# Optimization experiments

Measured on AMD Instinct MI355X. Metric: run time of the kernel, lower is better.

## Reference

```python
import jax, jax.numpy as jnp
import numpy as np

N = 100000   # nodes
E = 1600000  # edges
IN = 32      # in_dim
D = 64       # embed_dim
G = 128      # num graphs
EPS = 1e-5   # BatchNorm eps


def setup_inputs() -> dict:
    key = jax.random.key(0)
    ks = jax.random.split(key, 12)
    s_in = 1.0 / np.sqrt(IN)
    s_d = 1.0 / np.sqrt(D)
    return {
        "x": jax.random.normal(ks[0], (N, IN), jnp.float32),
        "edge_index": jax.random.randint(ks[1], (2, E), 0, N),
        "batch": jnp.sort(jax.random.randint(ks[2], (N,), 0, G)),
        "W_embed": jax.random.normal(ks[3], (IN, D), jnp.float32) * s_in,
        "W1": jax.random.normal(ks[4], (D, D), jnp.float32) * s_d,
        "b1": jnp.zeros((D,), jnp.float32),
        "g1": jnp.ones((D,), jnp.float32),
        "bt1": jnp.zeros((D,), jnp.float32),
        "W2": jax.random.normal(ks[5], (D, D), jnp.float32) * s_d,
        "b2": jnp.zeros((D,), jnp.float32),
        "g2": jnp.ones((D,), jnp.float32),
        "bt2": jnp.zeros((D,), jnp.float32),
    }


def reference(x, edge_index, batch, W_embed, W1, b1, g1, bt1, W2, b2, g2, bt2):
    src, dst = edge_index[0], edge_index[1]
    # GCN symmetric norm with self loops: deg = in-degree + 1 (self loop)
    deg = jnp.zeros((N,), x.dtype).at[dst].add(1.0) + 1.0
    dis = jax.lax.rsqrt(deg)                      # deg^{-1/2}, [N]
    enorm = dis[src] * dis[dst]                   # per-edge norm, [E]
    self_norm = dis * dis                         # self-loop norm, [N]

    def gcn_bn(h, W, b, g, bt, relu):
        hw = h @ W                                # linear first (GCNConv)
        msg = hw[src] * enorm[:, None]            # [E, D] gather + scale
        agg = jax.ops.segment_sum(msg, dst, num_segments=N)
        agg = agg + hw * self_norm[:, None] + b   # self loops + bias
        # BatchNorm1d (training mode: batch stats, biased var)
        mu = agg.mean(axis=0)
        var = agg.var(axis=0)
        hn = (agg - mu) * jax.lax.rsqrt(var + EPS) * g + bt
        return jnp.maximum(hn, 0.0) if relu else hn

    h = x @ W_embed                               # node_embed (Linear, no bias)
    h = gcn_bn(h, W1, b1, g1, bt1, relu=True)     # ReLU only between layers
    h = gcn_bn(h, W2, b2, g2, bt2, relu=False)
    h_pool = jax.ops.segment_sum(h, batch, num_segments=G)  # global_add_pool
    return (h, h_pool)
```

## Files before the change

kernel.cpp:

```cpp
#include <hip/hip_runtime.h>

#define NN 100000
#define NE 1600000
#define IN_DIM 32
#define DD 64
#define NG 128
#define BN_EPS 1e-5f
#define AGG_BLOCKS 2048

typedef unsigned short ushort_t;
typedef unsigned int uint_t;
typedef __attribute__((ext_vector_type(8))) short bf16x8;
typedef __attribute__((ext_vector_type(4))) float f32x4;

__device__ __forceinline__ ushort_t f2bf(float f) {
    uint_t u = __float_as_uint(f);
    u = (u + 0x7FFFu + ((u >> 16) & 1u)) >> 16;
    return (ushort_t)u;
}
__device__ __forceinline__ uint_t pack2(float a, float b) {
    return (uint_t)f2bf(a) | ((uint_t)f2bf(b) << 16);
}
__device__ __forceinline__ float bflo(uint_t u) { return __uint_as_float(u << 16); }
__device__ __forceinline__ float bfhi(uint_t u) { return __uint_as_float(u & 0xFFFF0000u); }

__global__ void init_k(int* __restrict__ ints, long n_ints, float* __restrict__ pool,
                       float* __restrict__ sums) {
    long i = (long)blockIdx.x * blockDim.x + threadIdx.x;
    if (i < n_ints) ints[i] = 0;
    if (i < (long)NG * DD) pool[i] = 0.f;
    if (i < 256) sums[i] = 0.f;
}

__global__ void deg_rank(const int* __restrict__ dst, int* __restrict__ cnt,
                         int* __restrict__ rank) {
    int e = blockIdx.x * blockDim.x + threadIdx.x;
    if (e < NE) rank[e] = atomicAdd(&cnt[dst[e]], 1);
}

__global__ __launch_bounds__(256) void alloc_k(const int* __restrict__ cnt,
                                               int* __restrict__ start,
                                               int* __restrict__ cursor,
                                               float* __restrict__ dis) {
    __shared__ int ls[256];
    __shared__ int base_s;
    int t = threadIdx.x;
    long n = (long)blockIdx.x * 256 + t;
    int v = (n < NN) ? cnt[n] : 0;
    ls[t] = v;
    __syncthreads();
    for (int off = 1; off < 256; off <<= 1) {
        int y = (t >= off) ? ls[t - off] : 0;
        __syncthreads();
        ls[t] += y;
        __syncthreads();
    }
    if (t == 0) base_s = atomicAdd(cursor, ls[255]);
    __syncthreads();
    if (n < NN) {
        start[n] = base_s + ls[t] - v;
        dis[n] = rsqrtf((float)v + 1.0f);
    }
}

__global__ void fill_edges(const int* __restrict__ src, const int* __restrict__ dstp,
                           const int* __restrict__ rank, const float* __restrict__ dis,
                           const int* __restrict__ start, uint_t* __restrict__ ep) {
    int e = blockIdx.x * blockDim.x + threadIdx.x;
    if (e >= NE) return;
    int s = src[e], t = dstp[e];
    float nm = dis[s] * dis[t];
    uint_t nb = (__float_as_uint(nm) + 0x8000u) >> 16;
    ep[start[t] + rank[e]] = (uint_t)s | ((nb & 0x7FFFu) << 17);
}

__global__ __launch_bounds__(256) void mm1_k(const float* __restrict__ x,
                                             const float* __restrict__ We,
                                             const float* __restrict__ W1,
                                             ushort_t* __restrict__ hwb) {
    __shared__ float W1s[DD * DD];
    __shared__ float Ws[IN_DIM * DD];
    int t = threadIdx.x;
    for (int i = t; i < DD * DD; i += 256) W1s[i] = W1[i];
    __syncthreads();
    for (int idx = t; idx < IN_DIM * DD; idx += 256) {
        int i = idx >> 6, j = idx & 63;
        float s = 0.f;
#pragma unroll
        for (int k = 0; k < DD; ++k) s += We[i * DD + k] * W1s[k * DD + j];
        Ws[idx] = s;
    }
    __syncthreads();
    long n = (long)blockIdx.x * 256 + t;
    if (n >= NN) return;
    float acc[DD];
#pragma unroll
    for (int d = 0; d < DD; ++d) acc[d] = 0.f;
    const float4* xr = (const float4*)(x + n * IN_DIM);
#pragma unroll
    for (int k4 = 0; k4 < IN_DIM / 4; ++k4) {
        float4 xv = xr[k4];
        const float* xp = (const float*)&xv;
#pragma unroll
        for (int kk = 0; kk < 4; ++kk) {
            float v = xp[kk];
            const float4* w4 = (const float4*)&Ws[(k4 * 4 + kk) * DD];
#pragma unroll
            for (int d4 = 0; d4 < DD / 4; ++d4) {
                float4 wv = w4[d4];
                acc[4 * d4 + 0] += v * wv.x;
                acc[4 * d4 + 1] += v * wv.y;
                acc[4 * d4 + 2] += v * wv.z;
                acc[4 * d4 + 3] += v * wv.w;
            }
        }
    }
    uint4* o = (uint4*)(hwb + n * DD);
#pragma unroll
    for (int d8 = 0; d8 < DD / 8; ++d8) {
        uint4 pk;
        pk.x = pack2(acc[8 * d8 + 0], acc[8 * d8 + 1]);
        pk.y = pack2(acc[8 * d8 + 2], acc[8 * d8 + 3]);
        pk.z = pack2(acc[8 * d8 + 4], acc[8 * d8 + 5]);
        pk.w = pack2(acc[8 * d8 + 6], acc[8 * d8 + 7]);
        o[d8] = pk;
    }
}

__global__ __launch_bounds__(256) void mm2_bn_mfma(const ushort_t* __restrict__ aggb,
                                                   const float* __restrict__ sums,
                                                   const float* __restrict__ g,
                                                   const float* __restrict__ bt,
                                                   const float* __restrict__ W,
                                                   ushort_t* __restrict__ hwb) {
    __shared__ ushort_t Wf[2 * 4 * 64 * 8];
    __shared__ float mu_s[DD], sc_s[DD], bt_s[DD];
    int t = threadIdx.x;
    if (t < DD) {
        const float inv_n = 1.0f / (float)NN;
        float mu = sums[t] * inv_n;
        float var = sums[64 + t] * inv_n - mu * mu;
        mu_s[t] = mu;
        sc_s[t] = g[t] * rsqrtf(var + BN_EPS);
        bt_s[t] = bt[t];
    }
    for (int e = t; e < 4096; e += 256) {
        int ks = e >> 11;
        int c = (e >> 9) & 3;
        int l = (e >> 3) & 63;
        int j = e & 7;
        int k = ks * 32 + ((l >> 4) << 3) + j;
        int col = c * 16 + (l & 15);
        Wf[e] = f2bf(W[k * DD + col]);
    }
    __syncthreads();

    int w = t >> 6, l = t & 63;
    int lr = l & 15, lk = l >> 4;

#pragma unroll
    for (int gi = 0; gi < 4; ++gi) {
        long rowbase = (long)blockIdx.x * 256 + w * 64 + gi * 16;
        long r = rowbase + lr;

        bf16x8 afrag[2];
#pragma unroll
        for (int ks = 0; ks < 2; ++ks) {
            int k0 = ks * 32 + (lk << 3);
            uint4 av = (r < NN) ? *(const uint4*)(aggb + r * DD + k0)
                                : make_uint4(0, 0, 0, 0);
            float4 muA = *(const float4*)&mu_s[k0];
            float4 muB = *(const float4*)&mu_s[k0 + 4];
            float4 scA = *(const float4*)&sc_s[k0];
            float4 scB = *(const float4*)&sc_s[k0 + 4];
            float4 btA = *(const float4*)&bt_s[k0];
            float4 btB = *(const float4*)&bt_s[k0 + 4];
            float h0 = fmaxf((bflo(av.x) - muA.x) * scA.x + btA.x, 0.f);
            float h1 = fmaxf((bfhi(av.x) - muA.y) * scA.y + btA.y, 0.f);
            float h2 = fmaxf((bflo(av.y) - muA.z) * scA.z + btA.z, 0.f);
            float h3 = fmaxf((bfhi(av.y) - muA.w) * scA.w + btA.w, 0.f);
            float h4 = fmaxf((bflo(av.z) - muB.x) * scB.x + btB.x, 0.f);
            float h5 = fmaxf((bfhi(av.z) - muB.y) * scB.y + btB.y, 0.f);
            float h6 = fmaxf((bflo(av.w) - muB.z) * scB.z + btB.z, 0.f);
            float h7 = fmaxf((bfhi(av.w) - muB.w) * scB.w + btB.w, 0.f);
            bf16x8 fr;
            fr[0] = (short)f2bf(h0); fr[1] = (short)f2bf(h1);
            fr[2] = (short)f2bf(h2); fr[3] = (short)f2bf(h3);
            fr[4] = (short)f2bf(h4); fr[5] = (short)f2bf(h5);
            fr[6] = (short)f2bf(h6); fr[7] = (short)f2bf(h7);
            afrag[ks] = fr;
        }

        f32x4 acc[4];
#pragma unroll
        for (int c = 0; c < 4; ++c) acc[c] = (f32x4){0.f, 0.f, 0.f, 0.f};
#pragma unroll
        for (int c = 0; c < 4; ++c) {
#pragma unroll
            for (int ks = 0; ks < 2; ++ks) {
                bf16x8 bfr = *(bf16x8*)&Wf[((ks * 4 + c) << 9) + (l << 3)];
                acc[c] = __builtin_amdgcn_mfma_f32_16x16x32_bf16(afrag[ks], bfr, acc[c],
                                                                 0, 0, 0);
            }
        }

#pragma unroll
        for (int c = 0; c < 4; ++c) {
#pragma unroll
            for (int rr = 0; rr < 4; ++rr) {
                long orow = rowbase + lk * 4 + rr;
                if (orow < NN) hwb[orow * DD + c * 16 + lr] = f2bf(acc[c][rr]);
            }
        }
    }
}

template <int WAGG_BF16>
__global__ __launch_bounds__(256) void gcn_agg(const ushort_t* __restrict__ hwb,
                                               const float* __restrict__ dis,
                                               const int* __restrict__ cnt,
                                               const int* __restrict__ start,
                                               const uint_t* __restrict__ ep,
                                               const float* __restrict__ bias,
                                               void* __restrict__ aggv,
                                               float* __restrict__ sums) {
    int t = threadIdx.x;
    int w = t >> 6;
    int lane = t & 63;
    int j = lane >> 3;
    int c = lane & 7;
    float selfmask = (j == 0) ? 1.f : 0.f;

    __shared__ float ls[4][128];
    for (int k = t; k < 512; k += 256) ((float*)ls)[k] = 0.f;
    __syncthreads();

    float bs[8];
#pragma unroll
    for (int k = 0; k < 8; ++k) bs[k] = bias[8 * c + k];

    for (long n = (long)blockIdx.x * 4 + w; n < NN; n += (long)gridDim.x * 4) {
        int rs = start[n];
        int ce = cnt[n];
        float sn = dis[n];
        float sq = sn * sn;

        uint4 sv = ((const uint4*)(hwb + (long)n * DD))[c];
        float acc[8];
        acc[0] = selfmask * (bflo(sv.x) * sq + bs[0]);
        acc[1] = selfmask * (bfhi(sv.x) * sq + bs[1]);
        acc[2] = selfmask * (bflo(sv.y) * sq + bs[2]);
        acc[3] = selfmask * (bfhi(sv.y) * sq + bs[3]);
        acc[4] = selfmask * (bflo(sv.z) * sq + bs[4]);
        acc[5] = selfmask * (bfhi(sv.z) * sq + bs[5]);
        acc[6] = selfmask * (bflo(sv.w) * sq + bs[6]);
        acc[7] = selfmask * (bfhi(sv.w) * sq + bs[7]);

        for (int i = 0; i < ce; i += 32) {
            int i0 = i + j, i1 = i + 8 + j, i2 = i + 16 + j, i3 = i + 24 + j;
            uint_t u0 = (i0 < ce) ? ep[rs + i0] : 0u;
            uint_t u1 = (i1 < ce) ? ep[rs + i1] : 0u;
            uint_t u2 = (i2 < ce) ? ep[rs + i2] : 0u;
            uint_t u3 = (i3 < ce) ? ep[rs + i3] : 0u;
            uint4 q0 = ((const uint4*)(hwb + (long)(u0 & 0x1FFFF) * DD))[c];
            uint4 q1 = ((const uint4*)(hwb + (long)(u1 & 0x1FFFF) * DD))[c];
            uint4 q2 = ((const uint4*)(hwb + (long)(u2 & 0x1FFFF) * DD))[c];
            uint4 q3 = ((const uint4*)(hwb + (long)(u3 & 0x1FFFF) * DD))[c];
            float n0 = __uint_as_float((u0 >> 17) << 16);
            float n1 = __uint_as_float((u1 >> 17) << 16);
            float n2 = __uint_as_float((u2 >> 17) << 16);
            float n3 = __uint_as_float((u3 >> 17) << 16);
            acc[0] += bflo(q0.x) * n0; acc[1] += bfhi(q0.x) * n0;
            acc[2] += bflo(q0.y) * n0; acc[3] += bfhi(q0.y) * n0;
            acc[4] += bflo(q0.z) * n0; acc[5] += bfhi(q0.z) * n0;
            acc[6] += bflo(q0.w) * n0; acc[7] += bfhi(q0.w) * n0;
            acc[0] += bflo(q1.x) * n1; acc[1] += bfhi(q1.x) * n1;
            acc[2] += bflo(q1.y) * n1; acc[3] += bfhi(q1.y) * n1;
            acc[4] += bflo(q1.z) * n1; acc[5] += bfhi(q1.z) * n1;
            acc[6] += bflo(q1.w) * n1; acc[7] += bfhi(q1.w) * n1;
            acc[0] += bflo(q2.x) * n2; acc[1] += bfhi(q2.x) * n2;
            acc[2] += bflo(q2.y) * n2; acc[3] += bfhi(q2.y) * n2;
            acc[4] += bflo(q2.z) * n2; acc[5] += bfhi(q2.z) * n2;
            acc[6] += bflo(q2.w) * n2; acc[7] += bfhi(q2.w) * n2;
            acc[0] += bflo(q3.x) * n3; acc[1] += bfhi(q3.x) * n3;
            acc[2] += bflo(q3.y) * n3; acc[3] += bfhi(q3.y) * n3;
            acc[4] += bflo(q3.z) * n3; acc[5] += bfhi(q3.z) * n3;
            acc[6] += bflo(q3.w) * n3; acc[7] += bfhi(q3.w) * n3;
        }

#pragma unroll
        for (int m = 8; m < 64; m <<= 1) {
#pragma unroll
            for (int k = 0; k < 8; ++k) acc[k] += __shfl_xor(acc[k], m, 64);
        }

        if (j == 0) {
            if (WAGG_BF16) {
                uint4 pk;
                pk.x = pack2(acc[0], acc[1]);
                pk.y = pack2(acc[2], acc[3]);
                pk.z = pack2(acc[4], acc[5]);
                pk.w = pack2(acc[6], acc[7]);
                ((uint4*)((ushort_t*)aggv + (long)n * DD))[c] = pk;
            } else {
                float4* op = (float4*)((float*)aggv + (long)n * DD + 8 * c);
                op[0] = make_float4(acc[0], acc[1], acc[2], acc[3]);
                op[1] = make_float4(acc[4], acc[5], acc[6], acc[7]);
            }
#pragma unroll
            for (int k = 0; k < 8; ++k) {
                ls[w][8 * c + k] += acc[k];
                ls[w][64 + 8 * c + k] += acc[k] * acc[k];
            }
        }
    }

    __syncthreads();
    if (t < 128) {
        float a = ls[0][t] + ls[1][t] + ls[2][t] + ls[3][t];
        atomicAdd(&sums[t], a);
    }
}

__global__ __launch_bounds__(256) void bn_pool(const float* __restrict__ agg,
                                               const float* __restrict__ sums,
                                               const float* __restrict__ g,
                                               const float* __restrict__ bt,
                                               const int* __restrict__ batch,
                                               float* __restrict__ out,
                                               float* __restrict__ pool) {
    int t = threadIdx.x;
    int d = t & 63, rq = t >> 6;
    const float inv_n = 1.0f / (float)NN;
    float mu = sums[d] * inv_n;
    float var = sums[64 + d] * inv_n - mu * mu;
    float sc = g[d] * rsqrtf(var + BN_EPS);
    float bd = bt[d];
    long base = (long)blockIdx.x * 256;
    float acc = 0.f;
    int cur = -1;
    for (int i = 0; i < 64; ++i) {
        long r = base + rq + 4 * i;
        if (r >= NN) break;
        int b = batch[r];
        float v = (agg[r * DD + d] - mu) * sc + bd;
        out[r * DD + d] = v;
        if (b != cur) {
            if (cur >= 0) atomicAdd(&pool[(long)cur * DD + d], acc);
            acc = 0.f;
            cur = b;
        }
        acc += v;
    }
    if (cur >= 0) atomicAdd(&pool[(long)cur * DD + d], acc);
}

extern "C" void kernel_launch(void* const* d_in, const int* in_sizes, int n_in,
                              void* d_out, int out_size, void* d_ws, size_t ws_size,
                              hipStream_t stream) {
    const float* x = (const float*)d_in[0];
    const int* ei = (const int*)d_in[1];
    const int* batch = (const int*)d_in[2];
    const float* W_embed = (const float*)d_in[3];
    const float* W1 = (const float*)d_in[4];
    const float* b1 = (const float*)d_in[5];
    const float* g1 = (const float*)d_in[6];
    const float* bt1 = (const float*)d_in[7];
    const float* W2 = (const float*)d_in[8];
    const float* b2 = (const float*)d_in[9];
    const float* g2 = (const float*)d_in[10];
    const float* bt2 = (const float*)d_in[11];

    const int* src = ei;
    const int* dst = ei + NE;

    float* out = (float*)d_out;
    float* pool = out + (long)NN * DD;

    const long ND = (long)NN * DD;

    char* w = (char*)d_ws;
    int* cnt = (int*)w;           w += sizeof(int) * NN;
    int* cursor = (int*)w;        w += sizeof(int) * 4;
    int* start = (int*)w;         w += sizeof(int) * NN;
    float* dis = (float*)w;       w += sizeof(float) * NN;
    float* sums1 = (float*)w;     w += sizeof(float) * 128;
    float* sums2 = (float*)w;     w += sizeof(float) * 128;
    int* rank = (int*)w;          w += sizeof(int) * NE;
    uint_t* ep = (uint_t*)w;      w += sizeof(uint_t) * NE;
    ushort_t* hwb = (ushort_t*)w; w += sizeof(ushort_t) * ND;
    ushort_t* agg1b = (ushort_t*)w; w += sizeof(ushort_t) * ND;
    float* aggbuf = (float*)w;

    dim3 blk(256);
    const int nbN = (NN + 255) / 256;
    const int nbE = (NE + 255) / 256;
    const long n_ints = (long)NN + 4;

    init_k<<<dim3((int)((n_ints + 255) / 256)), blk, 0, stream>>>(cnt, n_ints, pool, sums1);
    deg_rank<<<dim3(nbE), blk, 0, stream>>>(dst, cnt, rank);
    alloc_k<<<dim3(nbN), blk, 0, stream>>>(cnt, start, cursor, dis);
    fill_edges<<<dim3(nbE), blk, 0, stream>>>(src, dst, rank, dis, start, ep);

    mm1_k<<<dim3(nbN), blk, 0, stream>>>(x, W_embed, W1, hwb);

    gcn_agg<1><<<dim3(AGG_BLOCKS), blk, 0, stream>>>(hwb, dis, cnt, start, ep, b1,
                                                     (void*)agg1b, sums1);

    mm2_bn_mfma<<<dim3(nbN), blk, 0, stream>>>(agg1b, sums1, g1, bt1, W2, hwb);

    gcn_agg<0><<<dim3(AGG_BLOCKS), blk, 0, stream>>>(hwb, dis, cnt, start, ep, b2,
                                                     (void*)aggbuf, sums2);

    bn_pool<<<dim3(nbN), blk, 0, stream>>>(aggbuf, sums2, g2, bt2, batch, out, pool);
}
```

Baseline: 401.2 us.

## Factor GCN symmetric norm into pre/post scaling and drop per-edge weights

Folds dis[src] into the stored node features (scaled in mm1 and mm2 epilogues) and applies dis[dst] once per destination after aggregation, so each edge needs no per-edge norm. The edge list becomes plain source indices, fill_edges no longer gathers dis, and the inner aggregation loop loses its per-edge multiplies and bit-unpacking. Out-of-range lanes now point at an extra zeroed padding row instead of row 0. Rounding changes slightly because the scaled features are stored in bf16 before summation.

```diff
diff --git a/kernel.cpp b/kernel.cpp
--- a/kernel.cpp
+++ b/kernel.cpp
@@ -25,11 +25,12 @@
 __device__ __forceinline__ float bfhi(uint_t u) { return __uint_as_float(u & 0xFFFF0000u); }
 
 __global__ void init_k(int* __restrict__ ints, long n_ints, float* __restrict__ pool,
-                       float* __restrict__ sums) {
+                       float* __restrict__ sums, ushort_t* __restrict__ hwb) {
     long i = (long)blockIdx.x * blockDim.x + threadIdx.x;
     if (i < n_ints) ints[i] = 0;
     if (i < (long)NG * DD) pool[i] = 0.f;
     if (i < 256) sums[i] = 0.f;
+    if (i < DD) hwb[(long)NN * DD + i] = 0;
 }
 
 __global__ void deg_rank(const int* __restrict__ dst, int* __restrict__ cnt,
@@ -64,19 +65,17 @@
 }
 
 __global__ void fill_edges(const int* __restrict__ src, const int* __restrict__ dstp,
-                           const int* __restrict__ rank, const float* __restrict__ dis,
-                           const int* __restrict__ start, uint_t* __restrict__ ep) {
+                           const int* __restrict__ rank, const int* __restrict__ start,
+                           int* __restrict__ ep) {
     int e = blockIdx.x * blockDim.x + threadIdx.x;
     if (e >= NE) return;
-    int s = src[e], t = dstp[e];
-    float nm = dis[s] * dis[t];
-    uint_t nb = (__float_as_uint(nm) + 0x8000u) >> 16;
-    ep[start[t] + rank[e]] = (uint_t)s | ((nb & 0x7FFFu) << 17);
+    ep[start[dstp[e]] + rank[e]] = src[e];
 }
 
 __global__ __launch_bounds__(256) void mm1_k(const float* __restrict__ x,
                                              const float* __restrict__ We,
                                              const float* __restrict__ W1,
+                                             const float* __restrict__ dis,
                                              ushort_t* __restrict__ hwb) {
     __shared__ float W1s[DD * DD];
     __shared__ float Ws[IN_DIM * DD];
@@ -115,14 +114,15 @@
             }
         }
     }
+    float sn = dis[n];
     uint4* o = (uint4*)(hwb + n * DD);
 #pragma unroll
     for (int d8 = 0; d8 < DD / 8; ++d8) {
         uint4 pk;
-        pk.x = pack2(acc[8 * d8 + 0], acc[8 * d8 + 1]);
-        pk.y = pack2(acc[8 * d8 + 2], acc[8 * d8 + 3]);
-        pk.z = pack2(acc[8 * d8 + 4], acc[8 * d8 + 5]);
-        pk.w = pack2(acc[8 * d8 + 6], acc[8 * d8 + 7]);
+        pk.x = pack2(acc[8 * d8 + 0] * sn, acc[8 * d8 + 1] * sn);
+        pk.y = pack2(acc[8 * d8 + 2] * sn, acc[8 * d8 + 3] * sn);
+        pk.z = pack2(acc[8 * d8 + 4] * sn, acc[8 * d8 + 5] * sn);
+        pk.w = pack2(acc[8 * d8 + 6] * sn, acc[8 * d8 + 7] * sn);
         o[d8] = pk;
     }
 }
@@ -132,6 +132,7 @@
                                                    const float* __restrict__ g,
                                                    const float* __restrict__ bt,
                                                    const float* __restrict__ W,
+                                                   const float* __restrict__ dis,
                                                    ushort_t* __restrict__ hwb) {
     __shared__ ushort_t Wf[2 * 4 * 64 * 8];
     __shared__ float mu_s[DD], sc_s[DD], bt_s[DD];
@@ -205,11 +206,13 @@
         }
 
 #pragma unroll
-        for (int c = 0; c < 4; ++c) {
-#pragma unroll
-            for (int rr = 0; rr < 4; ++rr) {
-                long orow = rowbase + lk * 4 + rr;
-                if (orow < NN) hwb[orow * DD + c * 16 + lr] = f2bf(acc[c][rr]);
+        for (int rr = 0; rr < 4; ++rr) {
+            long orow = rowbase + lk * 4 + rr;
+            if (orow < NN) {
+                float sn = dis[orow];
+#pragma unroll
+                for (int c = 0; c < 4; ++c)
+                    hwb[orow * DD + c * 16 + lr] = f2bf(acc[c][rr] * sn);
             }
         }
     }
@@ -220,7 +223,7 @@
                                                const float* __restrict__ dis,
                                                const int* __restrict__ cnt,
                                                const int* __restrict__ start,
-                                               const uint_t* __restrict__ ep,
+                                               const int* __restrict__ ep,
                                                const float* __restrict__ bias,
                                                void* __restrict__ aggv,
                                                float* __restrict__ sums) {
@@ -242,50 +245,44 @@
     for (long n = (long)blockIdx.x * 4 + w; n < NN; n += (long)gridDim.x * 4) {
         int rs = start[n];
         int ce = cnt[n];
-        float sn = dis[n];
-        float sq = sn * sn;
 
         uint4 sv = ((const uint4*)(hwb + (long)n * DD))[c];
         float acc[8];
-        acc[0] = selfmask * (bflo(sv.x) * sq + bs[0]);
-        acc[1] = selfmask * (bfhi(sv.x) * sq + bs[1]);
-        acc[2] = selfmask * (bflo(sv.y) * sq + bs[2]);
-        acc[3] = selfmask * (bfhi(sv.y) * sq + bs[3]);
-        acc[4] = selfmask * (bflo(sv.z) * sq + bs[4]);
-        acc[5] = selfmask * (bfhi(sv.z) * sq + bs[5]);
-        acc[6] = selfmask * (bflo(sv.w) * sq + bs[6]);
-        acc[7] = selfmask * (bfhi(sv.w) * sq + bs[7]);
+        acc[0] = selfmask * bflo(sv.x);
+        acc[1] = selfmask * bfhi(sv.x);
+        acc[2] = selfmask * bflo(sv.y);
+        acc[3] = selfmask * bfhi(sv.y);
+        acc[4] = selfmask * bflo(sv.z);
+        acc[5] = selfmask * bfhi(sv.z);
+        acc[6] = selfmask * bflo(sv.w);
+        acc[7] = selfmask * bfhi(sv.w);
 
         for (int i = 0; i < ce; i += 32) {
             int i0 = i + j, i1 = i + 8 + j, i2 = i + 16 + j, i3 = i + 24 + j;
-            uint_t u0 = (i0 < ce) ? ep[rs + i0] : 0u;
-            uint_t u1 = (i1 < ce) ? ep[rs + i1] : 0u;
-            uint_t u2 = (i2 < ce) ? ep[rs + i2] : 0u;
-            uint_t u3 = (i3 < ce) ? ep[rs + i3] : 0u;
-            uint4 q0 = ((const uint4*)(hwb + (long)(u0 & 0x1FFFF) * DD))[c];
-            uint4 q1 = ((const uint4*)(hwb + (long)(u1 & 0x1FFFF) * DD))[c];
-            uint4 q2 = ((const uint4*)(hwb + (long)(u2 & 0x1FFFF) * DD))[c];
-            uint4 q3 = ((const uint4*)(hwb + (long)(u3 & 0x1FFFF) * DD))[c];
-            float n0 = __uint_as_float((u0 >> 17) << 16);
-            float n1 = __uint_as_float((u1 >> 17) << 16);
-            float n2 = __uint_as_float((u2 >> 17) << 16);
-            float n3 = __uint_as_float((u3 >> 17) << 16);
-            acc[0] += bflo(q0.x) * n0; acc[1] += bfhi(q0.x) * n0;
-            acc[2] += bflo(q0.y) * n0; acc[3] += bfhi(q0.y) * n0;
-            acc[4] += bflo(q0.z) * n0; acc[5] += bfhi(q0.z) * n0;
-            acc[6] += bflo(q0.w) * n0; acc[7] += bfhi(q0.w) * n0;
-            acc[0] += bflo(q1.x) * n1; acc[1] += bfhi(q1.x) * n1;
-            acc[2] += bflo(q1.y) * n1; acc[3] += bfhi(q1.y) * n1;
-            acc[4] += bflo(q1.z) * n1; acc[5] += bfhi(q1.z) * n1;
-            acc[6] += bflo(q1.w) * n1; acc[7] += bfhi(q1.w) * n1;
-            acc[0] += bflo(q2.x) * n2; acc[1] += bfhi(q2.x) * n2;
-            acc[2] += bflo(q2.y) * n2; acc[3] += bfhi(q2.y) * n2;
-            acc[4] += bflo(q2.z) * n2; acc[5] += bfhi(q2.z) * n2;
-            acc[6] += bflo(q2.w) * n2; acc[7] += bfhi(q2.w) * n2;
-            acc[0] += bflo(q3.x) * n3; acc[1] += bfhi(q3.x) * n3;
-            acc[2] += bflo(q3.y) * n3; acc[3] += bfhi(q3.y) * n3;
-            acc[4] += bflo(q3.z) * n3; acc[5] += bfhi(q3.z) * n3;
-            acc[6] += bflo(q3.w) * n3; acc[7] += bfhi(q3.w) * n3;
+            int u0 = (i0 < ce) ? ep[rs + i0] : NN;
+            int u1 = (i1 < ce) ? ep[rs + i1] : NN;
+            int u2 = (i2 < ce) ? ep[rs + i2] : NN;
+            int u3 = (i3 < ce) ? ep[rs + i3] : NN;
+            uint4 q0 = ((const uint4*)(hwb + (long)u0 * DD))[c];
+            uint4 q1 = ((const uint4*)(hwb + (long)u1 * DD))[c];
+            uint4 q2 = ((const uint4*)(hwb + (long)u2 * DD))[c];
+            uint4 q3 = ((const uint4*)(hwb + (long)u3 * DD))[c];
+            acc[0] += bflo(q0.x); acc[1] += bfhi(q0.x);
+            acc[2] += bflo(q0.y); acc[3] += bfhi(q0.y);
+            acc[4] += bflo(q0.z); acc[5] += bfhi(q0.z);
+            acc[6] += bflo(q0.w); acc[7] += bfhi(q0.w);
+            acc[0] += bflo(q1.x); acc[1] += bfhi(q1.x);
+            acc[2] += bflo(q1.y); acc[3] += bfhi(q1.y);
+            acc[4] += bflo(q1.z); acc[5] += bfhi(q1.z);
+            acc[6] += bflo(q1.w); acc[7] += bfhi(q1.w);
+            acc[0] += bflo(q2.x); acc[1] += bfhi(q2.x);
+            acc[2] += bflo(q2.y); acc[3] += bfhi(q2.y);
+            acc[4] += bflo(q2.z); acc[5] += bfhi(q2.z);
+            acc[6] += bflo(q2.w); acc[7] += bfhi(q2.w);
+            acc[0] += bflo(q3.x); acc[1] += bfhi(q3.x);
+            acc[2] += bflo(q3.y); acc[3] += bfhi(q3.y);
+            acc[4] += bflo(q3.z); acc[5] += bfhi(q3.z);
+            acc[6] += bflo(q3.w); acc[7] += bfhi(q3.w);
         }
 
 #pragma unroll
@@ -295,22 +292,26 @@
         }
 
         if (j == 0) {
+            float sn = dis[n];
+            float v[8];
+#pragma unroll
+            for (int k = 0; k < 8; ++k) v[k] = acc[k] * sn + bs[k];
             if (WAGG_BF16) {
                 uint4 pk;
-                pk.x = pack2(acc[0], acc[1]);
-                pk.y = pack2(acc[2], acc[3]);
-                pk.z = pack2(acc[4], acc[5]);
-                pk.w = pack2(acc[6], acc[7]);
+                pk.x = pack2(v[0], v[1]);
+                pk.y = pack2(v[2], v[3]);
+                pk.z = pack2(v[4], v[5]);
+                pk.w = pack2(v[6], v[7]);
                 ((uint4*)((ushort_t*)aggv + (long)n * DD))[c] = pk;
             } else {
                 float4* op = (float4*)((float*)aggv + (long)n * DD + 8 * c);
-                op[0] = make_float4(acc[0], acc[1], acc[2], acc[3]);
-                op[1] = make_float4(acc[4], acc[5], acc[6], acc[7]);
+                op[0] = make_float4(v[0], v[1], v[2], v[3]);
+                op[1] = make_float4(v[4], v[5], v[6], v[7]);
             }
 #pragma unroll
             for (int k = 0; k < 8; ++k) {
-                ls[w][8 * c + k] += acc[k];
-                ls[w][64 + 8 * c + k] += acc[k] * acc[k];
+                ls[w][8 * c + k] += v[k];
+                ls[w][64 + 8 * c + k] += v[k] * v[k];
             }
         }
     }
@@ -387,8 +388,8 @@
     float* sums1 = (float*)w;     w += sizeof(float) * 128;
     float* sums2 = (float*)w;     w += sizeof(float) * 128;
     int* rank = (int*)w;          w += sizeof(int) * NE;
-    uint_t* ep = (uint_t*)w;      w += sizeof(uint_t) * NE;
-    ushort_t* hwb = (ushort_t*)w; w += sizeof(ushort_t) * ND;
+    int* ep = (int*)w;            w += sizeof(int) * NE;
+    ushort_t* hwb = (ushort_t*)w; w += sizeof(ushort_t) * (ND + DD);
     ushort_t* agg1b = (ushort_t*)w; w += sizeof(ushort_t) * ND;
     float* aggbuf = (float*)w;
 
@@ -397,17 +398,18 @@
     const int nbE = (NE + 255) / 256;
     const long n_ints = (long)NN + 4;
 
-    init_k<<<dim3((int)((n_ints + 255) / 256)), blk, 0, stream>>>(cnt, n_ints, pool, sums1);
+    init_k<<<dim3((int)((n_ints + 255) / 256)), blk, 0, stream>>>(cnt, n_ints, pool,
+                                                                  sums1, hwb);
     deg_rank<<<dim3(nbE), blk, 0, stream>>>(dst, cnt, rank);
     alloc_k<<<dim3(nbN), blk, 0, stream>>>(cnt, start, cursor, dis);
-    fill_edges<<<dim3(nbE), blk, 0, stream>>>(src, dst, rank, dis, start, ep);
-
-    mm1_k<<<dim3(nbN), blk, 0, stream>>>(x, W_embed, W1, hwb);
+    fill_edges<<<dim3(nbE), blk, 0, stream>>>(src, dst, rank, start, ep);
+
+    mm1_k<<<dim3(nbN), blk, 0, stream>>>(x, W_embed, W1, dis, hwb);
 
     gcn_agg<1><<<dim3(AGG_BLOCKS), blk, 0, stream>>>(hwb, dis, cnt, start, ep, b1,
                                                      (void*)agg1b, sums1);
 
-    mm2_bn_mfma<<<dim3(nbN), blk, 0, stream>>>(agg1b, sums1, g1, bt1, W2, hwb);
+    mm2_bn_mfma<<<dim3(nbN), blk, 0, stream>>>(agg1b, sums1, g1, bt1, W2, dis, hwb);
 
     gcn_agg<0><<<dim3(AGG_BLOCKS), blk, 0, stream>>>(hwb, dis, cnt, start, ep, b2,
                                                      (void*)aggbuf, sums2);
```

New measurement: 405.0 us. About the same (+0.9%).
